# Performance work log

Hardware: AMD Instinct MI355X
Metric: run time of the kernel (lower is better)

## Reference

```python
import jax, jax.numpy as jnp
import numpy as np

N = 32768
LATENT = 2
HID = 100
STEPS = 100

swish = jax.nn.swish


def setup_inputs() -> dict:
    key = jax.random.key(0)
    ks = jax.random.split(key, 12)

    def w(k, shape):
        fan_in = shape[0]
        return (jax.random.normal(k, shape) / np.sqrt(fan_in)).astype(jnp.float32)

    return {
        "x": jax.random.normal(ks[0], (N, 3), dtype=jnp.float32),
        # encoder: 3 -> 100 -> 100 -> (mu: 2, log_t: 1)
        "We1": w(ks[1], (3, HID)), "be1": jnp.zeros((HID,), jnp.float32),
        "We2": w(ks[2], (HID, HID)), "be2": jnp.zeros((HID,), jnp.float32),
        "Wmu": w(ks[3], (HID, LATENT)), "bmu": jnp.zeros((LATENT,), jnp.float32),
        "Wlt": w(ks[4], (HID, 1)), "blt": jnp.zeros((1,), jnp.float32),
        # decoder: 2 -> 100 -> (mu: 3, log_sigma: 3)
        "Wd1": w(ks[5], (LATENT, HID)), "bd1": jnp.zeros((HID,), jnp.float32),
        "Wdmu": w(ks[6], (HID, 3)), "bdmu": jnp.zeros((3,), jnp.float32),
        "Wds": w(ks[7], (HID, 3)), "bds": jnp.zeros((3,), jnp.float32),
        # prior layer biases
        "b_muz": jnp.zeros((LATENT,), jnp.float32),
        "b_ltz": jnp.zeros((1,), jnp.float32),
        # standard-normal noise for the 100-step SDE (dW = sqrt(dt) * noise)
        "noise": jax.random.normal(ks[8], (STEPS, N, LATENT), dtype=jnp.float32),
    }


def reference(x, We1, be1, We2, be2, Wmu, bmu, Wlt, blt,
              Wd1, bd1, Wdmu, bdmu, Wds, bds, b_muz, b_ltz, noise):
    x = x.astype(jnp.float32)

    # ---- decoder heads on a single latent point z: (LATENT,) ----
    def dec_mu(z):
        return swish(z @ Wd1 + bd1) @ Wdmu + bdmu      # (3,)

    def dec_ls(z):
        return swish(z @ Wd1 + bd1) @ Wds + bds        # (3,)

    def G(z):  # pullback metric, (LATENT, LATENT)
        Jmu = jax.jacfwd(dec_mu)(z)   # (3, LATENT)
        Jsg = jax.jacfwd(dec_ls)(z)   # (3, LATENT)
        return Jmu.T @ Jmu + Jsg.T @ Jsg

    def step_one(z, dW):  # one Euler-Maruyama step for one point
        g = G(z)
        ginv = jnp.linalg.inv(g)
        Dg = jax.jacfwd(G)(z)         # (LATENT, LATENT, LATENT): dG[k,m]/dz_l
        Chris = 0.5 * (jnp.einsum('im,kml->ikl', ginv, Dg)
                       + jnp.einsum('im,lmk->ikl', ginv, Dg)
                       - jnp.einsum('im,klm->ikl', ginv, Dg))
        det = 0.5 * jnp.einsum('jk,ijk->i', ginv, Chris)
        stoch = ginv @ dW
        return (z + det + stoch).astype(jnp.float32)

    # ---- encoder ----
    h = swish(x @ We1 + be1)
    h = swish(h @ We2 + be2)
    mu_zx = h @ Wmu + bmu            # (N, LATENT)
    log_t_zx = h @ Wlt + blt         # (N, 1)

    # ---- Riemannian Brownian-motion sampling (Local) ----
    t = jnp.exp(2.0 * log_t_zx)[:, 0]        # (N,)
    dt = t / STEPS                            # (N,), constant over steps
    dW = jnp.sqrt(dt)[None, :, None] * noise  # (STEPS, N, LATENT)

    def scan_step(z, dW_t):
        return jax.vmap(step_one)(z, dW_t), None

    z, _ = jax.lax.scan(scan_step, mu_zx, dW)

    # ---- prior + decoder outputs ----
    mu_z = b_muz * jnp.ones_like(z)
    log_t_z = b_ltz * jnp.ones((z.shape[0], 1), z.dtype)
    hz = swish(z @ Wd1 + bd1)
    mu_xz = hz @ Wdmu + bdmu
    log_sigma_xz = hz @ Wds + bds

    return (z, mu_xz, log_sigma_xz, mu_zx, log_t_zx, mu_z, log_t_z)
```

## Files before the change

kernel.cpp:

```cpp
#include <hip/hip_runtime.h>

#define N_PTS 32768
#define HID   100
#define STEPS 100
#define NPAIR 52
#define LPP   13

#define OFF_Z     0
#define OFF_MUXZ  65536
#define OFF_LSXZ  163840
#define OFF_MUZX  262144
#define OFF_LTZX  327680
#define OFF_MUZ   360448
#define OFF_LTZ   425984

typedef float v2f __attribute__((ext_vector_type(2)));
typedef float v4f __attribute__((ext_vector_type(4)));

#if __has_builtin(__builtin_elementwise_fma)
#define FMA2(a, b, c) __builtin_elementwise_fma((a), (b), (c))
#else
#define FMA2(a, b, c) ((a) * (b) + (c))
#endif
#define LOv(q) __builtin_shufflevector((q), (q), 0, 1)
#define HIv(q) __builtin_shufflevector((q), (q), 2, 3)

__device__ __forceinline__ v2f splat(float x) { v2f r; r.x = x; r.y = x; return r; }

__device__ __forceinline__ float qreduce(float v) {
  v += __int_as_float(__builtin_amdgcn_update_dpp(0, __float_as_int(v), 0xB1, 0xF, 0xF, true));
  v += __int_as_float(__builtin_amdgcn_update_dpp(0, __float_as_int(v), 0x4E, 0xF, 0xF, true));
  return v;
}
__device__ __forceinline__ float hqreduce(v2f v) { return qreduce(v.x + v.y); }

template<int NP>
__device__ __forceinline__ void enc_chunk(
    int ob, float x0, float x1, float x2,
    const float* __restrict__ We1, const float* __restrict__ be1,
    const float* __restrict__ We2, const float* __restrict__ be2,
    const float* __restrict__ Wmu, const float* __restrict__ Wlt,
    float& m0, float& m1, float& lt)
{
  v2f acc2[NP];
  #pragma unroll
  for (int i = 0; i < NP; ++i) acc2[i] = splat(0.f);

  #pragma unroll 2
  for (int k = 0; k < HID; k += 2) {
    const v2f w0 = *(const v2f*)(We1 + k);
    const v2f w1 = *(const v2f*)(We1 + HID + k);
    const v2f w2 = *(const v2f*)(We1 + 2*HID + k);
    const v2f bb = *(const v2f*)(be1 + k);
    v2f aP = FMA2(splat(x0), w0, FMA2(splat(x1), w1, FMA2(splat(x2), w2, bb)));
    const float e0 = __expf(-aP.x), e1 = __expf(-aP.y);
    const float s0 = 1.f / (1.f + e0), s1 = 1.f / (1.f + e1);
    const v2f hh0 = splat(aP.x * s0);
    const v2f hh1 = splat(aP.y * s1);
    const v2f* r0 = (const v2f*)(We2 + k*HID + ob);
    const v2f* r1 = (const v2f*)(We2 + (k+1)*HID + ob);
    #pragma unroll
    for (int oo = 0; oo < NP; ++oo) {
      v2f tacc = FMA2(hh0, r0[oo], acc2[oo]);
      acc2[oo] = FMA2(hh1, r1[oo], tacc);
    }
  }

  m0 = 0.f; m1 = 0.f; lt = 0.f;
  #pragma unroll
  for (int oo = 0; oo < NP; ++oo) {
    #pragma unroll
    for (int h = 0; h < 2; ++h) {
      const int o = ob + 2*oo + h;
      float a   = (h ? acc2[oo].y : acc2[oo].x) + be2[o];
      float sig = 1.f / (1.f + __expf(-a));
      float h2  = a * sig;
      m0 = fmaf(h2, Wmu[o*2+0], m0);
      m1 = fmaf(h2, Wmu[o*2+1], m1);
      lt = fmaf(h2, Wlt[o],     lt);
    }
  }
}

__global__ __launch_bounds__(256, 2) void enc_kernel(
    const float* __restrict__ x,
    const float* __restrict__ We1, const float* __restrict__ be1,
    const float* __restrict__ We2, const float* __restrict__ be2,
    const float* __restrict__ Wmu, const float* __restrict__ bmu,
    const float* __restrict__ Wlt, const float* __restrict__ blt,
    const float* __restrict__ b_muz, const float* __restrict__ b_ltz,
    float* __restrict__ out)
{
  const int tid = threadIdx.x;
  const int w   = tid >> 6;
  const int pb  = tid & 63;
  const int p   = blockIdx.x * 64 + pb;

  const float x0 = x[p*3+0], x1 = x[p*3+1], x2 = x[p*3+2];

  float m0, m1, lt;
  if (w < 2) enc_chunk<13>(w * 26,            x0, x1, x2, We1, be1, We2, be2, Wmu, Wlt, m0, m1, lt);
  else       enc_chunk<12>(52 + (w - 2) * 24, x0, x1, x2, We1, be1, We2, be2, Wmu, Wlt, m0, m1, lt);

  __shared__ float red[4][64][3];
  red[w][pb][0] = m0; red[w][pb][1] = m1; red[w][pb][2] = lt;
  __syncthreads();
  if (w == 0) {
    m0 += red[1][pb][0] + red[2][pb][0] + red[3][pb][0] + bmu[0];
    m1 += red[1][pb][1] + red[2][pb][1] + red[3][pb][1] + bmu[1];
    lt += red[1][pb][2] + red[2][pb][2] + red[3][pb][2] + blt[0];
    out[OFF_MUZX + p*2+0] = m0;
    out[OFF_MUZX + p*2+1] = m1;
    out[OFF_LTZX + p]     = lt;
    out[OFF_MUZ  + p*2+0] = b_muz[0];
    out[OFF_MUZ  + p*2+1] = b_muz[1];
    out[OFF_LTZ  + p]     = b_ltz[0];
  }
}

__global__ __launch_bounds__(256, 2) void sde_kernel(
    const float* __restrict__ Wd1,  const float* __restrict__ bd1,
    const float* __restrict__ Wdmu, const float* __restrict__ bdmu,
    const float* __restrict__ Wds,  const float* __restrict__ bds,
    const float* __restrict__ noise,
    float* __restrict__ out)
{
  __shared__ __align__(16) float wrec[NPAIR * 24];
  const int tid = threadIdx.x;
  for (int idx = tid; idx < NPAIR * 24; idx += 256) {
    const int pr = idx / 24, f = idx - pr * 24;
    const int j  = pr * 2 + (f & 1);
    const int g  = f >> 1;
    float v = 0.f;
    if (j < HID) {
      const float w0 = Wd1[j], w1 = Wd1[HID + j];
      switch (g) {
        case 0:  v = w0; break;
        case 1:  v = w1; break;
        case 2:  v = bd1[j]; break;
        case 3:  v = w1 * w1; break;
        case 4:  v = w0 * w0; break;
        case 5:  v = w0 * w1; break;
        case 6:  v = Wdmu[j*3+0]; break;
        case 7:  v = Wds [j*3+0]; break;
        case 8:  v = Wdmu[j*3+1]; break;
        case 9:  v = Wds [j*3+1]; break;
        case 10: v = Wdmu[j*3+2]; break;
        default: v = Wds [j*3+2]; break;
      }
    }
    wrec[idx] = v;
  }
  __syncthreads();

  const int l     = tid & 3;
  const int p     = blockIdx.x * 64 + (tid >> 2);
  const int pbase = l * LPP;
  const v4f* __restrict__ Rq = (const v4f*)wrec;

  float z0 = out[OFF_MUZX + p*2+0];
  float z1 = out[OFF_MUZX + p*2+1];
  const float sdt = __expf(out[OFF_LTZX + p]) * 0.1f;

  const float2* __restrict__ noise2 = (const float2*)noise;

  for (int step = 0; step < STEPS; ++step) {
    const float2 nz = noise2[(size_t)step * N_PTS + p];

    v2f Jm[3][2], Js[3][2], Km[3][3], Ks[3][3];
    #pragma unroll
    for (int o = 0; o < 3; ++o) {
      Jm[o][0]=splat(0.f); Jm[o][1]=splat(0.f);
      Js[o][0]=splat(0.f); Js[o][1]=splat(0.f);
      Km[o][0]=splat(0.f); Km[o][1]=splat(0.f); Km[o][2]=splat(0.f);
      Ks[o][0]=splat(0.f); Ks[o][1]=splat(0.f); Ks[o][2]=splat(0.f);
    }
    const v2f z0P = splat(z0), z1P = splat(z1);

    const v4f* R = Rq + pbase * 6;
    #pragma unroll 2
    for (int t = 0; t < LPP; ++t, R += 6) {
      const v4f A  = R[0];
      const v4f B  = R[1];
      const v4f Cq = R[2];
      const v4f M0 = R[3], M1 = R[4], M2 = R[5];
      const v2f W0P  = LOv(A),  W1P  = HIv(A);
      const v2f bP   = LOv(B),  W11P = HIv(B);
      const v2f W00P = LOv(Cq), W01P = HIv(Cq);

      v2f aP = FMA2(z0P, W0P, FMA2(z1P, W1P, bP));
      v2f eP;   eP.x   = __expf(-aP.x);               eP.y   = __expf(-aP.y);
      v2f dP = splat(1.f) + eP;
      v2f sigP; sigP.x = __builtin_amdgcn_rcpf(dP.x); sigP.y = __builtin_amdgcn_rcpf(dP.y);
      const v2f t1P = splat(1.f) - sigP;
      const v2f ppP = sigP * t1P;
      const v2f uP  = FMA2(aP, ppP, sigP);
      const v2f u2P = ppP * FMA2(aP, FMA2(splat(-2.f), sigP, splat(1.f)), splat(2.f));
      const v2f c0  = uP  * W0P,  c1  = uP  * W1P;
      const v2f q00 = u2P * W00P, q01 = u2P * W01P, q11 = u2P * W11P;

      const v2f mP0 = LOv(M0), mP1 = LOv(M1), mP2 = LOv(M2);
      const v2f sP0 = HIv(M0), sP1 = HIv(M1), sP2 = HIv(M2);

      Jm[0][0] = FMA2(c0,  mP0, Jm[0][0]);  Jm[0][1] = FMA2(c1,  mP0, Jm[0][1]);
      Js[0][0] = FMA2(c0,  sP0, Js[0][0]);  Js[0][1] = FMA2(c1,  sP0, Js[0][1]);
      Km[0][0] = FMA2(q00, mP0, Km[0][0]);  Km[0][1] = FMA2(q01, mP0, Km[0][1]);
      Km[0][2] = FMA2(q11, mP0, Km[0][2]);
      Ks[0][0] = FMA2(q00, sP0, Ks[0][0]);  Ks[0][1] = FMA2(q01, sP0, Ks[0][1]);
      Ks[0][2] = FMA2(q11, sP0, Ks[0][2]);

      Jm[1][0] = FMA2(c0,  mP1, Jm[1][0]);  Jm[1][1] = FMA2(c1,  mP1, Jm[1][1]);
      Js[1][0] = FMA2(c0,  sP1, Js[1][0]);  Js[1][1] = FMA2(c1,  sP1, Js[1][1]);
      Km[1][0] = FMA2(q00, mP1, Km[1][0]);  Km[1][1] = FMA2(q01, mP1, Km[1][1]);
      Km[1][2] = FMA2(q11, mP1, Km[1][2]);
      Ks[1][0] = FMA2(q00, sP1, Ks[1][0]);  Ks[1][1] = FMA2(q01, sP1, Ks[1][1]);
      Ks[1][2] = FMA2(q11, sP1, Ks[1][2]);

      Jm[2][0] = FMA2(c0,  mP2, Jm[2][0]);  Jm[2][1] = FMA2(c1,  mP2, Jm[2][1]);
      Js[2][0] = FMA2(c0,  sP2, Js[2][0]);  Js[2][1] = FMA2(c1,  sP2, Js[2][1]);
      Km[2][0] = FMA2(q00, mP2, Km[2][0]);  Km[2][1] = FMA2(q01, mP2, Km[2][1]);
      Km[2][2] = FMA2(q11, mP2, Km[2][2]);
      Ks[2][0] = FMA2(q00, sP2, Ks[2][0]);  Ks[2][1] = FMA2(q01, sP2, Ks[2][1]);
      Ks[2][2] = FMA2(q11, sP2, Ks[2][2]);
    }

    float JmS[3][2], JsS[3][2], KmS[3][3], KsS[3][3];
    #pragma unroll
    for (int o = 0; o < 3; ++o) {
      JmS[o][0]=hqreduce(Jm[o][0]); JmS[o][1]=hqreduce(Jm[o][1]);
      JsS[o][0]=hqreduce(Js[o][0]); JsS[o][1]=hqreduce(Js[o][1]);
      KmS[o][0]=hqreduce(Km[o][0]); KmS[o][1]=hqreduce(Km[o][1]); KmS[o][2]=hqreduce(Km[o][2]);
      KsS[o][0]=hqreduce(Ks[o][0]); KsS[o][1]=hqreduce(Ks[o][1]); KsS[o][2]=hqreduce(Ks[o][2]);
    }

    float G00=0.f, G01=0.f, G11=0.f;
    #pragma unroll
    for (int o = 0; o < 3; ++o) {
      G00 += JmS[o][0]*JmS[o][0] + JsS[o][0]*JsS[o][0];
      G01 += JmS[o][0]*JmS[o][1] + JsS[o][0]*JsS[o][1];
      G11 += JmS[o][1]*JmS[o][1] + JsS[o][1]*JsS[o][1];
    }
    float D00=0.f, D01=0.f, D10=0.f, D11=0.f, D20=0.f, D21=0.f;
    #pragma unroll
    for (int o = 0; o < 3; ++o) {
      D00 += 2.f*(KmS[o][0]*JmS[o][0] + KsS[o][0]*JsS[o][0]);
      D01 += 2.f*(KmS[o][1]*JmS[o][0] + KsS[o][1]*JsS[o][0]);
      D10 += KmS[o][0]*JmS[o][1] + JmS[o][0]*KmS[o][1] + KsS[o][0]*JsS[o][1] + JsS[o][0]*KsS[o][1];
      D11 += KmS[o][1]*JmS[o][1] + JmS[o][0]*KmS[o][2] + KsS[o][1]*JsS[o][1] + JsS[o][0]*KsS[o][2];
      D20 += 2.f*(KmS[o][1]*JmS[o][1] + KsS[o][1]*JsS[o][1]);
      D21 += 2.f*(KmS[o][2]*JmS[o][1] + KsS[o][2]*JsS[o][1]);
    }
    const float det = fmaf(G00, G11, -G01*G01);
    const float id  = __builtin_amdgcn_rcpf(det);
    const float i00 = G11*id, i01 = -G01*id, i11 = G00*id;
    const float T000 = D00;
    const float T001 = 2.f*D10 - D01;
    const float T010 = D01;
    const float T011 = D20;
    const float T110 = 2.f*D11 - D20;
    const float T111 = D21;
    const float C00 = 0.5f*(i00*T000 + i01*T001);
    const float C01 = 0.5f*(i00*T010 + i01*T011);
    const float C02 = 0.5f*(i00*T110 + i01*T111);
    const float C10 = 0.5f*(i01*T000 + i11*T001);
    const float C11 = 0.5f*(i01*T010 + i11*T011);
    const float C12 = 0.5f*(i01*T110 + i11*T111);
    const float dr0 = 0.5f*(i00*C00 + 2.f*i01*C01 + i11*C02);
    const float dr1 = 0.5f*(i00*C10 + 2.f*i01*C11 + i11*C12);

    const float dw0 = sdt*nz.x, dw1 = sdt*nz.y;
    z0 += dr0 + i00*dw0 + i01*dw1;
    z1 += dr1 + i01*dw0 + i11*dw1;
  }

  v2f MSm[3], MSs[3];
  #pragma unroll
  for (int o = 0; o < 3; ++o) { MSm[o] = splat(0.f); MSs[o] = splat(0.f); }
  const v2f zf0 = splat(z0), zf1 = splat(z1);
  {
    const v4f* R = Rq + pbase * 6;
    #pragma unroll 2
    for (int t = 0; t < LPP; ++t, R += 6) {
      const v4f A  = R[0];
      const v4f B  = R[1];
      const v4f M0 = R[3], M1 = R[4], M2 = R[5];
      v2f aP = FMA2(zf0, LOv(A), FMA2(zf1, HIv(A), LOv(B)));
      v2f eP;   eP.x   = __expf(-aP.x);               eP.y   = __expf(-aP.y);
      v2f dP = splat(1.f) + eP;
      v2f sigP; sigP.x = __builtin_amdgcn_rcpf(dP.x); sigP.y = __builtin_amdgcn_rcpf(dP.y);
      const v2f hP = aP * sigP;
      MSm[0] = FMA2(hP, LOv(M0), MSm[0]);  MSs[0] = FMA2(hP, HIv(M0), MSs[0]);
      MSm[1] = FMA2(hP, LOv(M1), MSm[1]);  MSs[1] = FMA2(hP, HIv(M1), MSs[1]);
      MSm[2] = FMA2(hP, LOv(M2), MSm[2]);  MSs[2] = FMA2(hP, HIv(M2), MSs[2]);
    }
  }
  float mu[3], ls[3];
  #pragma unroll
  for (int o = 0; o < 3; ++o) { mu[o] = hqreduce(MSm[o]); ls[o] = hqreduce(MSs[o]); }

  if (l == 0) {
    out[OFF_Z + p*2+0] = z0;
    out[OFF_Z + p*2+1] = z1;
    #pragma unroll
    for (int o = 0; o < 3; ++o) {
      out[OFF_MUXZ + p*3 + o] = mu[o] + bdmu[o];
      out[OFF_LSXZ + p*3 + o] = ls[o] + bds[o];
    }
  }
}

extern "C" void kernel_launch(void* const* d_in, const int* in_sizes, int n_in,
                              void* d_out, int out_size, void* d_ws, size_t ws_size,
                              hipStream_t stream) {
  (void)in_sizes; (void)n_in; (void)d_ws; (void)ws_size; (void)out_size;
  const float* x    = (const float*)d_in[0];
  const float* We1  = (const float*)d_in[1];
  const float* be1  = (const float*)d_in[2];
  const float* We2  = (const float*)d_in[3];
  const float* be2  = (const float*)d_in[4];
  const float* Wmu  = (const float*)d_in[5];
  const float* bmu  = (const float*)d_in[6];
  const float* Wlt  = (const float*)d_in[7];
  const float* blt  = (const float*)d_in[8];
  const float* Wd1  = (const float*)d_in[9];
  const float* bd1  = (const float*)d_in[10];
  const float* Wdmu = (const float*)d_in[11];
  const float* bdmu = (const float*)d_in[12];
  const float* Wds  = (const float*)d_in[13];
  const float* bds  = (const float*)d_in[14];
  const float* bmz  = (const float*)d_in[15];
  const float* blz  = (const float*)d_in[16];
  const float* noise= (const float*)d_in[17];
  float* out = (float*)d_out;

  enc_kernel<<<512, 256, 0, stream>>>(x, We1, be1, We2, be2, Wmu, bmu, Wlt, blt,
                                      bmz, blz, out);
  sde_kernel<<<512, 256, 0, stream>>>(Wd1, bd1, Wdmu, bdmu, Wds, bds, noise, out);
}
```

Measured before the change: 571.1 us.

## Fuse encoder and SDE kernels, simplify sigmoid derivatives and drift algebra

Merges the encoder and the SDE kernel into one launch. The encoder's mu and log_t are handed to the SDE loop through shared memory instead of being written to global memory and read back. Rewrites the second-derivative swish terms with fewer operations, collapses the Christoffel/drift contraction into a shorter FMA chain, and raises the inner loop unroll from 2 to 4. This saves one launch and a global round trip. In exchange the block does encoder work before the loop, and the wider unroll may raise register pressure.

```diff
diff --git a/kernel.cpp b/kernel.cpp
--- a/kernel.cpp
+++ b/kernel.cpp
@@ -82,51 +82,25 @@
   }
 }
 
-__global__ __launch_bounds__(256, 2) void enc_kernel(
+__global__ __launch_bounds__(256, 2) void vaebm_kernel(
     const float* __restrict__ x,
     const float* __restrict__ We1, const float* __restrict__ be1,
     const float* __restrict__ We2, const float* __restrict__ be2,
     const float* __restrict__ Wmu, const float* __restrict__ bmu,
     const float* __restrict__ Wlt, const float* __restrict__ blt,
-    const float* __restrict__ b_muz, const float* __restrict__ b_ltz,
-    float* __restrict__ out)
-{
-  const int tid = threadIdx.x;
-  const int w   = tid >> 6;
-  const int pb  = tid & 63;
-  const int p   = blockIdx.x * 64 + pb;
-
-  const float x0 = x[p*3+0], x1 = x[p*3+1], x2 = x[p*3+2];
-
-  float m0, m1, lt;
-  if (w < 2) enc_chunk<13>(w * 26,            x0, x1, x2, We1, be1, We2, be2, Wmu, Wlt, m0, m1, lt);
-  else       enc_chunk<12>(52 + (w - 2) * 24, x0, x1, x2, We1, be1, We2, be2, Wmu, Wlt, m0, m1, lt);
-
-  __shared__ float red[4][64][3];
-  red[w][pb][0] = m0; red[w][pb][1] = m1; red[w][pb][2] = lt;
-  __syncthreads();
-  if (w == 0) {
-    m0 += red[1][pb][0] + red[2][pb][0] + red[3][pb][0] + bmu[0];
-    m1 += red[1][pb][1] + red[2][pb][1] + red[3][pb][1] + bmu[1];
-    lt += red[1][pb][2] + red[2][pb][2] + red[3][pb][2] + blt[0];
-    out[OFF_MUZX + p*2+0] = m0;
-    out[OFF_MUZX + p*2+1] = m1;
-    out[OFF_LTZX + p]     = lt;
-    out[OFF_MUZ  + p*2+0] = b_muz[0];
-    out[OFF_MUZ  + p*2+1] = b_muz[1];
-    out[OFF_LTZ  + p]     = b_ltz[0];
-  }
-}
-
-__global__ __launch_bounds__(256, 2) void sde_kernel(
     const float* __restrict__ Wd1,  const float* __restrict__ bd1,
     const float* __restrict__ Wdmu, const float* __restrict__ bdmu,
     const float* __restrict__ Wds,  const float* __restrict__ bds,
+    const float* __restrict__ b_muz, const float* __restrict__ b_ltz,
     const float* __restrict__ noise,
     float* __restrict__ out)
 {
   __shared__ __align__(16) float wrec[NPAIR * 24];
+  __shared__ float red[4][64][3];
+  __shared__ float zlds[64][3];
+
   const int tid = threadIdx.x;
+
   for (int idx = tid; idx < NPAIR * 24; idx += 256) {
     const int pr = idx / 24, f = idx - pr * 24;
     const int j  = pr * 2 + (f & 1);
@@ -151,21 +125,47 @@
     }
     wrec[idx] = v;
   }
+
+  const int w  = tid >> 6;
+  const int pb = tid & 63;
+  const int p  = blockIdx.x * 64 + pb;
+
+  const float x0 = x[p*3+0], x1 = x[p*3+1], x2 = x[p*3+2];
+
+  float m0, m1, lt;
+  if (w < 2) enc_chunk<13>(w * 26,            x0, x1, x2, We1, be1, We2, be2, Wmu, Wlt, m0, m1, lt);
+  else       enc_chunk<12>(52 + (w - 2) * 24, x0, x1, x2, We1, be1, We2, be2, Wmu, Wlt, m0, m1, lt);
+
+  red[w][pb][0] = m0; red[w][pb][1] = m1; red[w][pb][2] = lt;
   __syncthreads();
+  if (w == 0) {
+    m0 += red[1][pb][0] + red[2][pb][0] + red[3][pb][0] + bmu[0];
+    m1 += red[1][pb][1] + red[2][pb][1] + red[3][pb][1] + bmu[1];
+    lt += red[1][pb][2] + red[2][pb][2] + red[3][pb][2] + blt[0];
+    out[OFF_MUZX + p*2+0] = m0;
+    out[OFF_MUZX + p*2+1] = m1;
+    out[OFF_LTZX + p]     = lt;
+    out[OFF_MUZ  + p*2+0] = b_muz[0];
+    out[OFF_MUZ  + p*2+1] = b_muz[1];
+    out[OFF_LTZ  + p]     = b_ltz[0];
+    zlds[pb][0] = m0; zlds[pb][1] = m1; zlds[pb][2] = lt;
+  }
+  __syncthreads();
 
   const int l     = tid & 3;
-  const int p     = blockIdx.x * 64 + (tid >> 2);
+  const int pt    = tid >> 2;
+  const int pg    = blockIdx.x * 64 + pt;
   const int pbase = l * LPP;
   const v4f* __restrict__ Rq = (const v4f*)wrec;
 
-  float z0 = out[OFF_MUZX + p*2+0];
-  float z1 = out[OFF_MUZX + p*2+1];
-  const float sdt = __expf(out[OFF_LTZX + p]) * 0.1f;
+  float z0 = zlds[pt][0];
+  float z1 = zlds[pt][1];
+  const float sdt = __expf(zlds[pt][2]) * 0.1f;
 
   const float2* __restrict__ noise2 = (const float2*)noise;
 
   for (int step = 0; step < STEPS; ++step) {
-    const float2 nz = noise2[(size_t)step * N_PTS + p];
+    const float2 nz = noise2[(size_t)step * N_PTS + pg];
 
     v2f Jm[3][2], Js[3][2], Km[3][3], Ks[3][3];
     #pragma unroll
@@ -178,7 +178,7 @@
     const v2f z0P = splat(z0), z1P = splat(z1);
 
     const v4f* R = Rq + pbase * 6;
-    #pragma unroll 2
+    #pragma unroll 4
     for (int t = 0; t < LPP; ++t, R += 6) {
       const v4f A  = R[0];
       const v4f B  = R[1];
@@ -192,10 +192,10 @@
       v2f eP;   eP.x   = __expf(-aP.x);               eP.y   = __expf(-aP.y);
       v2f dP = splat(1.f) + eP;
       v2f sigP; sigP.x = __builtin_amdgcn_rcpf(dP.x); sigP.y = __builtin_amdgcn_rcpf(dP.y);
-      const v2f t1P = splat(1.f) - sigP;
-      const v2f ppP = sigP * t1P;
-      const v2f uP  = FMA2(aP, ppP, sigP);
-      const v2f u2P = ppP * FMA2(aP, FMA2(splat(-2.f), sigP, splat(1.f)), splat(2.f));
+      const v2f ppP  = FMA2(-sigP, sigP, sigP);
+      const v2f uP   = FMA2(aP, ppP, sigP);
+      const v2f w2sP = FMA2(splat(-2.f), sigP, splat(1.f));
+      const v2f u2P  = FMA2(uP, w2sP, sigP);
       const v2f c0  = uP  * W0P,  c1  = uP  * W1P;
       const v2f q00 = u2P * W00P, q01 = u2P * W01P, q11 = u2P * W11P;
 
@@ -253,20 +253,15 @@
     const float det = fmaf(G00, G11, -G01*G01);
     const float id  = __builtin_amdgcn_rcpf(det);
     const float i00 = G11*id, i01 = -G01*id, i11 = G00*id;
-    const float T000 = D00;
-    const float T001 = 2.f*D10 - D01;
-    const float T010 = D01;
-    const float T011 = D20;
-    const float T110 = 2.f*D11 - D20;
-    const float T111 = D21;
-    const float C00 = 0.5f*(i00*T000 + i01*T001);
-    const float C01 = 0.5f*(i00*T010 + i01*T011);
-    const float C02 = 0.5f*(i00*T110 + i01*T111);
-    const float C10 = 0.5f*(i01*T000 + i11*T001);
-    const float C11 = 0.5f*(i01*T010 + i11*T011);
-    const float C12 = 0.5f*(i01*T110 + i11*T111);
-    const float dr0 = 0.5f*(i00*C00 + 2.f*i01*C01 + i11*C02);
-    const float dr1 = 0.5f*(i00*C10 + 2.f*i01*C11 + i11*C12);
+    const float S0 = fmaf(i00, D00, fmaf(i01, D01 + D10, i11 * D11));
+    const float S1 = fmaf(i00, D10, fmaf(i01, D11 + D20, i11 * D21));
+    const float i01d = i01 + i01;
+    const float P0 = fmaf(i00, D00, fmaf(i01d, D10, i11 * D20));
+    const float P1 = fmaf(i00, D01, fmaf(i01d, D11, i11 * D21));
+    const float R0 = fmaf(0.5f, S0, -0.25f * P0);
+    const float R1 = fmaf(0.5f, S1, -0.25f * P1);
+    const float dr0 = fmaf(i00, R0, i01 * R1);
+    const float dr1 = fmaf(i01, R0, i11 * R1);
 
     const float dw0 = sdt*nz.x, dw1 = sdt*nz.y;
     z0 += dr0 + i00*dw0 + i01*dw1;
@@ -299,12 +294,12 @@
   for (int o = 0; o < 3; ++o) { mu[o] = hqreduce(MSm[o]); ls[o] = hqreduce(MSs[o]); }
 
   if (l == 0) {
-    out[OFF_Z + p*2+0] = z0;
-    out[OFF_Z + p*2+1] = z1;
-    #pragma unroll
-    for (int o = 0; o < 3; ++o) {
-      out[OFF_MUXZ + p*3 + o] = mu[o] + bdmu[o];
-      out[OFF_LSXZ + p*3 + o] = ls[o] + bds[o];
+    out[OFF_Z + pg*2+0] = z0;
+    out[OFF_Z + pg*2+1] = z1;
+    #pragma unroll
+    for (int o = 0; o < 3; ++o) {
+      out[OFF_MUXZ + pg*3 + o] = mu[o] + bdmu[o];
+      out[OFF_LSXZ + pg*3 + o] = ls[o] + bds[o];
     }
   }
 }
@@ -333,7 +328,7 @@
   const float* noise= (const float*)d_in[17];
   float* out = (float*)d_out;
 
-  enc_kernel<<<512, 256, 0, stream>>>(x, We1, be1, We2, be2, Wmu, bmu, Wlt, blt,
-                                      bmz, blz, out);
-  sde_kernel<<<512, 256, 0, stream>>>(Wd1, bd1, Wdmu, bdmu, Wds, bds, noise, out);
+  vaebm_kernel<<<512, 256, 0, stream>>>(x, We1, be1, We2, be2, Wmu, bmu, Wlt, blt,
+                                        Wd1, bd1, Wdmu, bdmu, Wds, bds,
+                                        bmz, blz, noise, out);
 }
```

New measurement: 574.0 us (median of 3 runs). Within noise of the previous version (+0.5%).

## Split each point across 8 lanes with padded LDS records and simplified Christoffel drift

Applied to the files above, without the earlier changes.

Each point's hidden-unit reduction now spans 8 lanes instead of 4, with 7 pairs per lane. The grid doubles to 1024 blocks and launch bounds rise to 4 blocks per CU. LDS weight records are padded to a 28-float (7 x float4) stride, and the reductions add a third DPP stage (row_shr-like 0x141). The sigmoid-derivative math and the Christoffel/drift algebra are refactored into fewer FMAs. This aims at more parallelism per step and less per-lane serial work, at the cost of extra reduction shuffles, padding work and register pressure under the tighter launch bound.

```diff
diff --git a/kernel.cpp b/kernel.cpp
--- a/kernel.cpp
+++ b/kernel.cpp
@@ -3,8 +3,9 @@
 #define N_PTS 32768
 #define HID   100
 #define STEPS 100
-#define NPAIR 52
-#define LPP   13
+#define NPAIR 56
+#define LPP   7
+#define RSTR  28
 
 #define OFF_Z     0
 #define OFF_MUXZ  65536
@@ -27,12 +28,17 @@
 
 __device__ __forceinline__ v2f splat(float x) { v2f r; r.x = x; r.y = x; return r; }
 
+template<int CTRL>
+__device__ __forceinline__ float dppadd(float v) {
+  return v + __int_as_float(__builtin_amdgcn_update_dpp(0, __float_as_int(v), CTRL, 0xF, 0xF, true));
+}
 __device__ __forceinline__ float qreduce(float v) {
-  v += __int_as_float(__builtin_amdgcn_update_dpp(0, __float_as_int(v), 0xB1, 0xF, 0xF, true));
-  v += __int_as_float(__builtin_amdgcn_update_dpp(0, __float_as_int(v), 0x4E, 0xF, 0xF, true));
-  return v;
-}
-__device__ __forceinline__ float hqreduce(v2f v) { return qreduce(v.x + v.y); }
+  v = dppadd<0xB1>(v); v = dppadd<0x4E>(v); return v;
+}
+__device__ __forceinline__ float oreduce(float v) {
+  v = dppadd<0xB1>(v); v = dppadd<0x4E>(v); v = dppadd<0x141>(v); return v;
+}
+__device__ __forceinline__ float horeduce(v2f v) { return oreduce(v.x + v.y); }
 
 template<int NP>
 __device__ __forceinline__ void enc_chunk(
@@ -118,43 +124,46 @@
   }
 }
 
-__global__ __launch_bounds__(256, 2) void sde_kernel(
+__global__ __launch_bounds__(256, 4) void sde_kernel(
     const float* __restrict__ Wd1,  const float* __restrict__ bd1,
     const float* __restrict__ Wdmu, const float* __restrict__ bdmu,
     const float* __restrict__ Wds,  const float* __restrict__ bds,
     const float* __restrict__ noise,
     float* __restrict__ out)
 {
-  __shared__ __align__(16) float wrec[NPAIR * 24];
+  __shared__ __align__(16) float wrec[NPAIR * RSTR];
   const int tid = threadIdx.x;
-  for (int idx = tid; idx < NPAIR * 24; idx += 256) {
-    const int pr = idx / 24, f = idx - pr * 24;
-    const int j  = pr * 2 + (f & 1);
-    const int g  = f >> 1;
+  for (int idx = tid; idx < NPAIR * RSTR; idx += 256) {
+    const int pr = idx / RSTR, f = idx - pr * RSTR;
     float v = 0.f;
-    if (j < HID) {
-      const float w0 = Wd1[j], w1 = Wd1[HID + j];
-      switch (g) {
-        case 0:  v = w0; break;
-        case 1:  v = w1; break;
-        case 2:  v = bd1[j]; break;
-        case 3:  v = w1 * w1; break;
-        case 4:  v = w0 * w0; break;
-        case 5:  v = w0 * w1; break;
-        case 6:  v = Wdmu[j*3+0]; break;
-        case 7:  v = Wds [j*3+0]; break;
-        case 8:  v = Wdmu[j*3+1]; break;
-        case 9:  v = Wds [j*3+1]; break;
-        case 10: v = Wdmu[j*3+2]; break;
-        default: v = Wds [j*3+2]; break;
+    if (f < 24) {
+      const int j = pr * 2 + (f & 1);
+      const int g = f >> 1;
+      if (j < HID) {
+        const float w0 = Wd1[j], w1 = Wd1[HID + j];
+        switch (g) {
+          case 0:  v = w0; break;
+          case 1:  v = w1; break;
+          case 2:  v = bd1[j]; break;
+          case 3:  v = w1 * w1; break;
+          case 4:  v = w0 * w0; break;
+          case 5:  v = w0 * w1; break;
+          case 6:  v = Wdmu[j*3+0]; break;
+          case 7:  v = Wds [j*3+0]; break;
+          case 8:  v = Wdmu[j*3+1]; break;
+          case 9:  v = Wds [j*3+1]; break;
+          case 10: v = Wdmu[j*3+2]; break;
+          default: v = Wds [j*3+2]; break;
+        }
       }
     }
     wrec[idx] = v;
   }
   __syncthreads();
 
-  const int l     = tid & 3;
-  const int p     = blockIdx.x * 64 + (tid >> 2);
+  const int l     = tid & 7;
+  const int pt    = tid >> 3;
+  const int p     = blockIdx.x * 32 + pt;
   const int pbase = l * LPP;
   const v4f* __restrict__ Rq = (const v4f*)wrec;
 
@@ -177,9 +186,9 @@
     }
     const v2f z0P = splat(z0), z1P = splat(z1);
 
-    const v4f* R = Rq + pbase * 6;
+    const v4f* R = Rq + pbase * 7;
     #pragma unroll 2
-    for (int t = 0; t < LPP; ++t, R += 6) {
+    for (int t = 0; t < LPP; ++t, R += 7) {
       const v4f A  = R[0];
       const v4f B  = R[1];
       const v4f Cq = R[2];
@@ -192,10 +201,10 @@
       v2f eP;   eP.x   = __expf(-aP.x);               eP.y   = __expf(-aP.y);
       v2f dP = splat(1.f) + eP;
       v2f sigP; sigP.x = __builtin_amdgcn_rcpf(dP.x); sigP.y = __builtin_amdgcn_rcpf(dP.y);
-      const v2f t1P = splat(1.f) - sigP;
-      const v2f ppP = sigP * t1P;
-      const v2f uP  = FMA2(aP, ppP, sigP);
-      const v2f u2P = ppP * FMA2(aP, FMA2(splat(-2.f), sigP, splat(1.f)), splat(2.f));
+      const v2f ppP  = FMA2(-sigP, sigP, sigP);
+      const v2f uP   = FMA2(aP, ppP, sigP);
+      const v2f w2sP = FMA2(splat(-2.f), sigP, splat(1.f));
+      const v2f u2P  = FMA2(uP, w2sP, sigP);
       const v2f c0  = uP  * W0P,  c1  = uP  * W1P;
       const v2f q00 = u2P * W00P, q01 = u2P * W01P, q11 = u2P * W11P;
 
@@ -227,10 +236,10 @@
     float JmS[3][2], JsS[3][2], KmS[3][3], KsS[3][3];
     #pragma unroll
     for (int o = 0; o < 3; ++o) {
-      JmS[o][0]=hqreduce(Jm[o][0]); JmS[o][1]=hqreduce(Jm[o][1]);
-      JsS[o][0]=hqreduce(Js[o][0]); JsS[o][1]=hqreduce(Js[o][1]);
-      KmS[o][0]=hqreduce(Km[o][0]); KmS[o][1]=hqreduce(Km[o][1]); KmS[o][2]=hqreduce(Km[o][2]);
-      KsS[o][0]=hqreduce(Ks[o][0]); KsS[o][1]=hqreduce(Ks[o][1]); KsS[o][2]=hqreduce(Ks[o][2]);
+      JmS[o][0]=horeduce(Jm[o][0]); JmS[o][1]=horeduce(Jm[o][1]);
+      JsS[o][0]=horeduce(Js[o][0]); JsS[o][1]=horeduce(Js[o][1]);
+      KmS[o][0]=horeduce(Km[o][0]); KmS[o][1]=horeduce(Km[o][1]); KmS[o][2]=horeduce(Km[o][2]);
+      KsS[o][0]=horeduce(Ks[o][0]); KsS[o][1]=horeduce(Ks[o][1]); KsS[o][2]=horeduce(Ks[o][2]);
     }
 
     float G00=0.f, G01=0.f, G11=0.f;
@@ -253,20 +262,15 @@
     const float det = fmaf(G00, G11, -G01*G01);
     const float id  = __builtin_amdgcn_rcpf(det);
     const float i00 = G11*id, i01 = -G01*id, i11 = G00*id;
-    const float T000 = D00;
-    const float T001 = 2.f*D10 - D01;
-    const float T010 = D01;
-    const float T011 = D20;
-    const float T110 = 2.f*D11 - D20;
-    const float T111 = D21;
-    const float C00 = 0.5f*(i00*T000 + i01*T001);
-    const float C01 = 0.5f*(i00*T010 + i01*T011);
-    const float C02 = 0.5f*(i00*T110 + i01*T111);
-    const float C10 = 0.5f*(i01*T000 + i11*T001);
-    const float C11 = 0.5f*(i01*T010 + i11*T011);
-    const float C12 = 0.5f*(i01*T110 + i11*T111);
-    const float dr0 = 0.5f*(i00*C00 + 2.f*i01*C01 + i11*C02);
-    const float dr1 = 0.5f*(i00*C10 + 2.f*i01*C11 + i11*C12);
+    const float S0 = fmaf(i00, D00, fmaf(i01, D01 + D10, i11 * D11));
+    const float S1 = fmaf(i00, D10, fmaf(i01, D11 + D20, i11 * D21));
+    const float i01d = i01 + i01;
+    const float P0 = fmaf(i00, D00, fmaf(i01d, D10, i11 * D20));
+    const float P1 = fmaf(i00, D01, fmaf(i01d, D11, i11 * D21));
+    const float R0 = fmaf(0.5f, S0, -0.25f * P0);
+    const float R1v = fmaf(0.5f, S1, -0.25f * P1);
+    const float dr0 = fmaf(i00, R0, i01 * R1v);
+    const float dr1 = fmaf(i01, R0, i11 * R1v);
 
     const float dw0 = sdt*nz.x, dw1 = sdt*nz.y;
     z0 += dr0 + i00*dw0 + i01*dw1;
@@ -278,9 +282,9 @@
   for (int o = 0; o < 3; ++o) { MSm[o] = splat(0.f); MSs[o] = splat(0.f); }
   const v2f zf0 = splat(z0), zf1 = splat(z1);
   {
-    const v4f* R = Rq + pbase * 6;
+    const v4f* R = Rq + pbase * 7;
     #pragma unroll 2
-    for (int t = 0; t < LPP; ++t, R += 6) {
+    for (int t = 0; t < LPP; ++t, R += 7) {
       const v4f A  = R[0];
       const v4f B  = R[1];
       const v4f M0 = R[3], M1 = R[4], M2 = R[5];
@@ -296,7 +300,7 @@
   }
   float mu[3], ls[3];
   #pragma unroll
-  for (int o = 0; o < 3; ++o) { mu[o] = hqreduce(MSm[o]); ls[o] = hqreduce(MSs[o]); }
+  for (int o = 0; o < 3; ++o) { mu[o] = horeduce(MSm[o]); ls[o] = horeduce(MSs[o]); }
 
   if (l == 0) {
     out[OFF_Z + p*2+0] = z0;
@@ -335,5 +339,5 @@
 
   enc_kernel<<<512, 256, 0, stream>>>(x, We1, be1, We2, be2, Wmu, bmu, Wlt, blt,
                                       bmz, blz, out);
-  sde_kernel<<<512, 256, 0, stream>>>(Wd1, bd1, Wdmu, bdmu, Wds, bds, noise, out);
-}
+  sde_kernel<<<1024, 256, 0, stream>>>(Wd1, bd1, Wdmu, bdmu, Wds, bds, noise, out);
+}
```

Result: slower. 944.7 us (+65.4%).
